# Optimization experiments

Hardware: AMD Instinct MI355X
Metric: run time of the kernel (lower is better)

Reference implementation:

```python
import jax, jax.numpy as jnp
import numpy as np

THRESHOLD = 2.0

def setup_inputs() -> dict:
    key = jax.random.key(0)
    x = jax.random.normal(key, (8, 2048, 16, 16), dtype=jnp.float32)
    return {"x": x}

def reference(x):
    eps = 1e-6
    B, N = x.shape[0], x.shape[1]
    feat_shape = x.shape[2:]
    xf = x.reshape(B, N, -1)                      # (B, N, D)
    D = xf.shape[-1]
    # Silverman-style bandwidth per batch
    sigma = jnp.std(xf, axis=1).mean(axis=1) + eps          # (B,)  unbiased=False
    h = (4.0 / (D + 2)) ** (1.0 / (D + 4)) * N ** (-1.0 / (D + 4)) * sigma + eps
    h = h[:, None]                                           # (B, 1)
    # pairwise mean-squared distance via the dot-product identity:
    # mean_d (xi - xj)^2 = (|xi|^2 + |xj|^2 - 2 xi.xj) / D
    sq = jnp.sum(xf * xf, axis=-1)                           # (B, N)
    dots = jnp.einsum('bnd,bmd->bnm', xf, xf)                # (B, N, N)
    Dmat = (sq[:, :, None] + sq[:, None, :] - 2.0 * dots) / D
    densities = jnp.exp(-Dmat / (2.0 * h[:, :, None] ** 2 + eps)).sum(axis=2)  # (B, N)
    mean = densities.mean(axis=1, keepdims=True)
    std = jnp.std(densities, axis=1, ddof=1, keepdims=True)  # torch.std unbiased
    mask = densities > (mean - THRESHOLD * std)              # (B, N) bool
    cnt = mask.sum(axis=1)                                   # (B,)
    s = jnp.einsum('bnd,bn->bd', xf, mask.astype(xf.dtype))  # masked sum
    denom = jnp.maximum(cnt, 1).astype(xf.dtype)[:, None]
    means = jnp.where(cnt[:, None] > 0, s / denom, jnp.zeros_like(s))
    return means.reshape((B,) + feat_shape)
```

## Files before the change

kernel.cpp:

```cpp
#include <hip/hip_runtime.h>
#include <math.h>

#define NB 8
#define NN 2048
#define ND 256

typedef _Float16 f16;
typedef f16 f16x8 __attribute__((ext_vector_type(8)));
typedef f16 f16x4 __attribute__((ext_vector_type(4)));
typedef float f32x4 __attribute__((ext_vector_type(4)));

static constexpr float EPS = 1e-6f;

__device__ __forceinline__ void gload16(const void* g, void* l) {
    __builtin_amdgcn_global_load_lds(
        (const __attribute__((address_space(1))) unsigned int*)g,
        (__attribute__((address_space(3))) unsigned int*)l, 16, 0, 0);
}

__global__ __launch_bounds__(256) void k_prep(const float* __restrict__ x,
                                              f16* __restrict__ xh, f16* __restrict__ xl,
                                              float* __restrict__ partS,
                                              float* __restrict__ partSS,
                                              float* __restrict__ sq) {
    int b = blockIdx.y, ch = blockIdx.x;
    int t = threadIdx.x;
    int c = t & 63, rg = t >> 6;
    size_t base = ((size_t)b * NN + (size_t)ch * 64) * ND;
    float s0 = 0.f, s1 = 0.f, s2 = 0.f, s3 = 0.f;
    float q0 = 0.f, q1 = 0.f, q2 = 0.f, q3 = 0.f;
    for (int r = rg; r < 64; r += 4) {
        float4 v = *(const float4*)&x[base + (size_t)r * ND + c * 4];
        s0 += v.x; s1 += v.y; s2 += v.z; s3 += v.w;
        float p = v.x * v.x + v.y * v.y + v.z * v.z + v.w * v.w;
        q0 += v.x * v.x; q1 += v.y * v.y; q2 += v.z * v.z; q3 += v.w * v.w;
        f16 h0 = (f16)v.x, h1 = (f16)v.y, h2 = (f16)v.z, h3 = (f16)v.w;
        f16x4 hv = {h0, h1, h2, h3};
        f16x4 lv = {(f16)(v.x - (float)h0), (f16)(v.y - (float)h1),
                    (f16)(v.z - (float)h2), (f16)(v.w - (float)h3)};
        *(f16x4*)&xh[base + (size_t)r * ND + c * 4] = hv;
        *(f16x4*)&xl[base + (size_t)r * ND + c * 4] = lv;
        #pragma unroll
        for (int off = 32; off > 0; off >>= 1) p += __shfl_xor(p, off, 64);
        if (c == 0) sq[b * NN + ch * 64 + r] = p;
    }
    __shared__ float rS[4][64][4];
    __shared__ float rQ[4][64][4];
    rS[rg][c][0] = s0; rS[rg][c][1] = s1; rS[rg][c][2] = s2; rS[rg][c][3] = s3;
    rQ[rg][c][0] = q0; rQ[rg][c][1] = q1; rQ[rg][c][2] = q2; rQ[rg][c][3] = q3;
    __syncthreads();
    if (rg == 0) {
        #pragma unroll
        for (int e = 0; e < 4; ++e) {
            float S = rS[0][c][e] + rS[1][c][e] + rS[2][c][e] + rS[3][c][e];
            float Q = rQ[0][c][e] + rQ[1][c][e] + rQ[2][c][e] + rQ[3][c][e];
            partS[(b * 32 + ch) * ND + c * 4 + e] = S;
            partSS[(b * 32 + ch) * ND + c * 4 + e] = Q;
        }
    }
}

__global__ __launch_bounds__(256) void k_scale(const float* __restrict__ partS,
                                               const float* __restrict__ partSS,
                                               const float* __restrict__ sq,
                                               float* __restrict__ scale,
                                               float* __restrict__ em) {
    int b = blockIdx.x, d = threadIdx.x;
    float s = 0.f, ss = 0.f;
    for (int ch = 0; ch < 32; ++ch) {
        s += partS[(b * 32 + ch) * ND + d];
        ss += partSS[(b * 32 + ch) * ND + d];
    }
    float mean = s * (1.0f / NN);
    float var = ss * (1.0f / NN) - mean * mean;
    float sd = sqrtf(fmaxf(var, 0.f));
    __shared__ float red[256];
    __shared__ float s_sc;
    red[d] = sd;
    __syncthreads();
    for (int off = 128; off > 0; off >>= 1) {
        if (d < off) red[d] += red[d + off];
        __syncthreads();
    }
    if (d == 0) {
        float sigma = red[0] * (1.0f / ND) + EPS;
        double c = pow(4.0 / (ND + 2), 1.0 / (ND + 4)) * pow((double)NN, -1.0 / (ND + 4));
        float h = (float)c * sigma + EPS;
        s_sc = 1.0f / ((float)ND * (2.0f * h * h + EPS));
        scale[b] = s_sc;
    }
    __syncthreads();
    float sc = s_sc;
    for (int n = d; n < NN; n += 256) em[b * NN + n] = __expf(-sq[b * NN + n] * sc);
}

__global__ __launch_bounds__(256, 3) void k_dens(const f16* __restrict__ xh,
                                                 const f16* __restrict__ xl,
                                                 const float* __restrict__ em,
                                                 const float* __restrict__ scale,
                                                 float* __restrict__ dens_part) {
    int wg = blockIdx.x;
    int b = wg & 7;
    int t = wg >> 3;
    int ti = 0, basec = 0;
    while (t >= basec + (16 - ti)) { basec += 16 - ti; ++ti; }
    int tj = ti + (t - basec);
    int n0 = ti * 128;
    int m0 = tj * 128;

    int tid = threadIdx.x;
    int w = tid >> 6, lane = tid & 63;
    int wr = w >> 1, wc = w & 1;

    __shared__ alignas(16) f16 sAh[128 * 64];
    __shared__ alignas(16) f16 sBh[128 * 64];
    __shared__ alignas(16) f16 sBl[128 * 64];
    __shared__ float dl[2][128];
    __shared__ float dc[2][128];

    const size_t xb = (size_t)b * NN * ND;
    const f16* gAh = xh + xb + (size_t)n0 * ND;
    const f16* gBh = xh + xb + (size_t)m0 * ND;
    const f16* gBl = xl + xb + (size_t)m0 * ND;

    int offA[4], offB[4];
    #pragma unroll
    for (int i = 0; i < 4; ++i) {
        int rA = wr * 64 + i * 16 + (lane & 15);
        offA[i] = rA * 128 + ((((lane >> 4) ^ (rA & 7))) << 4);
        int rB = wc * 64 + i * 16 + (lane & 15);
        offB[i] = rB * 128 + ((((lane >> 4) ^ (rB & 7))) << 4);
    }

    f32x4 acc[4][4];
    #pragma unroll
    for (int i = 0; i < 4; ++i)
        #pragma unroll
        for (int j = 0; j < 4; ++j)
            acc[i][j] = (f32x4){0.f, 0.f, 0.f, 0.f};

    for (int kt = 0; kt < ND / 64; ++kt) {
        int k0 = kt * 64;
        #pragma unroll
        for (int p = 0; p < 4; ++p) {
            int f = p * 256 + w * 64 + lane;
            int row = f >> 3;
            int c = f & 7;
            int col = ((c ^ (row & 7)) << 3);
            size_t go = (size_t)row * ND + k0 + col;
            int lo = p * 2048 + w * 512;
            gload16(gAh + go, sAh + lo);
            gload16(gBh + go, sBh + lo);
            gload16(gBl + go, sBl + lo);
        }
        __syncthreads();

        #pragma unroll
        for (int kk = 0; kk < 2; ++kk) {
            int dx = kk << 6;
            f16x8 ah[4], bh[4], bl[4];
            #pragma unroll
            for (int i = 0; i < 4; ++i) {
                ah[i] = *(const f16x8*)((const char*)sAh + (offA[i] ^ dx));
                bh[i] = *(const f16x8*)((const char*)sBh + (offB[i] ^ dx));
                bl[i] = *(const f16x8*)((const char*)sBl + (offB[i] ^ dx));
            }
            #pragma unroll
            for (int i = 0; i < 4; ++i)
                #pragma unroll
                for (int j = 0; j < 4; ++j) {
                    acc[i][j] = __builtin_amdgcn_mfma_f32_16x16x32_f16(ah[i], bh[j], acc[i][j], 0, 0, 0);
                    acc[i][j] = __builtin_amdgcn_mfma_f32_16x16x32_f16(ah[i], bl[j], acc[i][j], 0, 0, 0);
                }
        }
        __syncthreads();
    }

    float sc2 = 2.0f * scale[b];
    float emv[4];
    #pragma unroll
    for (int j = 0; j < 4; ++j)
        emv[j] = em[b * NN + m0 + wc * 64 + j * 16 + (lane & 15)];
    float emn[4][4];
    #pragma unroll
    for (int i = 0; i < 4; ++i) {
        float4 v = *(const float4*)&em[b * NN + n0 + wr * 64 + i * 16 + (lane >> 4) * 4];
        emn[i][0] = v.x; emn[i][1] = v.y; emn[i][2] = v.z; emn[i][3] = v.w;
    }

    float colsum[4] = {0.f, 0.f, 0.f, 0.f};
    #pragma unroll
    for (int i = 0; i < 4; ++i)
        #pragma unroll
        for (int e = 0; e < 4; ++e) {
            float rs = 0.f;
            #pragma unroll
            for (int j = 0; j < 4; ++j) {
                float v = __expf(sc2 * acc[i][j][e]);
                rs += emv[j] * v;
                colsum[j] += emn[i][e] * v;
            }
            rs += __shfl_xor(rs, 1, 64);
            rs += __shfl_xor(rs, 2, 64);
            rs += __shfl_xor(rs, 4, 64);
            rs += __shfl_xor(rs, 8, 64);
            if ((lane & 15) == 0)
                dl[wc][wr * 64 + i * 16 + (lane >> 4) * 4 + e] = rs;
        }
    #pragma unroll
    for (int j = 0; j < 4; ++j) {
        float cs = colsum[j];
        cs += __shfl_xor(cs, 16, 64);
        cs += __shfl_xor(cs, 32, 64);
        if ((lane >> 4) == 0)
            dc[wr][wc * 64 + j * 16 + (lane & 15)] = cs;
    }
    __syncthreads();
    if (tid < 128) {
        dens_part[((size_t)(b * 16) + tj) * NN + n0 + tid] = dl[0][tid] + dl[1][tid];
    } else if (ti != tj) {
        int c = tid - 128;
        dens_part[((size_t)(b * 16) + ti) * NN + m0 + c] = dc[0][c] + dc[1][c];
    }
}

__global__ __launch_bounds__(256) void k_maskstat(const float* __restrict__ x,
                                                  const float* __restrict__ part,
                                                  const float* __restrict__ em,
                                                  float* __restrict__ partM,
                                                  int* __restrict__ partC) {
    int b = blockIdx.y, ch = blockIdx.x;
    int t = threadIdx.x;
    int c = t & 63, rg = t >> 6;

    float dloc[8];
    float s = 0.f;
    #pragma unroll
    for (int i = 0; i < 8; ++i) {
        int n = t + i * 256;
        float v = 0.f;
        #pragma unroll
        for (int mt = 0; mt < 16; ++mt) v += part[((size_t)(b * 16 + mt)) * NN + n];
        v *= em[b * NN + n];
        dloc[i] = v;
        s += v;
    }
    __shared__ float red[256];
    __shared__ float s_thr;
    __shared__ float sD[128];
    red[t] = s;
    __syncthreads();
    for (int off = 128; off > 0; off >>= 1) {
        if (t < off) red[t] += red[t + off];
        __syncthreads();
    }
    float mean = red[0] * (1.0f / NN);
    __syncthreads();
    float vs = 0.f;
    #pragma unroll
    for (int i = 0; i < 8; ++i) {
        float d2 = dloc[i] - mean;
        vs += d2 * d2;
    }
    red[t] = vs;
    {
        int i0 = ch >> 1;
        int tlo = (ch & 1) * 128;
        if (t >= tlo && t < tlo + 128) sD[t - tlo] = dloc[i0];
    }
    __syncthreads();
    for (int off = 128; off > 0; off >>= 1) {
        if (t < off) red[t] += red[t + off];
        __syncthreads();
    }
    if (t == 0) s_thr = mean - 2.0f * sqrtf(red[0] / (float)(NN - 1));
    __syncthreads();
    float tv = s_thr;

    float s0 = 0.f, s1 = 0.f, s2 = 0.f, s3 = 0.f;
    int cnt = 0;
    for (int r = rg; r < 128; r += 4) {
        int n = ch * 128 + r;
        if (sD[r] > tv) {
            float4 v = *(const float4*)&x[((size_t)b * NN + n) * ND + c * 4];
            s0 += v.x; s1 += v.y; s2 += v.z; s3 += v.w;
            ++cnt;
        }
    }
    __shared__ float rS[4][64][4];
    __shared__ int rC[4];
    rS[rg][c][0] = s0; rS[rg][c][1] = s1; rS[rg][c][2] = s2; rS[rg][c][3] = s3;
    if (c == 0) rC[rg] = cnt;
    __syncthreads();
    if (rg == 0) {
        #pragma unroll
        for (int e = 0; e < 4; ++e) {
            float S = rS[0][c][e] + rS[1][c][e] + rS[2][c][e] + rS[3][c][e];
            partM[(b * 16 + ch) * ND + c * 4 + e] = S;
        }
        if (c == 0) partC[b * 16 + ch] = rC[0] + rC[1] + rC[2] + rC[3];
    }
}

__global__ __launch_bounds__(256) void k_out(const float* __restrict__ partM,
                                             const int* __restrict__ partC,
                                             float* __restrict__ out) {
    int b = blockIdx.x, d = threadIdx.x;
    float s = 0.f;
    int cnt = 0;
    for (int ch = 0; ch < 16; ++ch) {
        s += partM[(b * 16 + ch) * ND + d];
        cnt += partC[b * 16 + ch];
    }
    out[b * ND + d] = (cnt > 0) ? s / (float)max(cnt, 1) : 0.f;
}

extern "C" void kernel_launch(void* const* d_in, const int* in_sizes, int n_in,
                              void* d_out, int out_size, void* d_ws, size_t ws_size,
                              hipStream_t stream) {
    const float* x = (const float*)d_in[0];
    float* out = (float*)d_out;

    char* p = (char*)d_ws;
    f16* xh = (f16*)p;            p += (size_t)NB * NN * ND * 2;
    f16* xl = (f16*)p;            p += (size_t)NB * NN * ND * 2;
    float* sq = (float*)p;        p += (size_t)NB * NN * 4;
    float* em = (float*)p;        p += (size_t)NB * NN * 4;
    float* partS = (float*)p;     p += (size_t)NB * 32 * ND * 4;
    float* partSS = (float*)p;    p += (size_t)NB * 32 * ND * 4;
    float* scale = (float*)p;     p += 256;
    float* dens_part = (float*)p; p += (size_t)NB * 16 * NN * 4;
    float* partM = (float*)p;     p += (size_t)NB * 16 * ND * 4;
    int* partC = (int*)p;         p += (size_t)NB * 16 * 4;

    k_prep<<<dim3(32, NB), 256, 0, stream>>>(x, xh, xl, partS, partSS, sq);
    k_scale<<<NB, 256, 0, stream>>>(partS, partSS, sq, scale, em);
    k_dens<<<136 * NB, 256, 0, stream>>>(xh, xl, em, scale, dens_part);
    k_maskstat<<<dim3(16, NB), 256, 0, stream>>>(x, dens_part, em, partM, partC);
    k_out<<<NB, 256, 0, stream>>>(partM, partC, out);
}
```

Baseline: 66.67 us.

## Fold bandwidth/scale kernel into consumers and fuse final reduction via last-block atomic

Removes the separate k_scale and k_out launches. Every density and mask-stat workgroup now recomputes the per-batch bandwidth scale from the partial sums and evaluates exp(-sq*scale) inline. The final per-batch mean is produced by the last-arriving k_maskstat block, chosen through an atomic counter that k_prep resets. This saves two launches and their serialization gaps. The cost is redundant reduction work in each of the 1088 density workgroups and extra synchronization inside k_dens.

```diff
diff --git a/kernel.cpp b/kernel.cpp
--- a/kernel.cpp
+++ b/kernel.cpp
@@ -11,6 +11,7 @@
 typedef float f32x4 __attribute__((ext_vector_type(4)));
 
 static constexpr float EPS = 1e-6f;
+static constexpr float CCONST = 0.95566186f;
 
 __device__ __forceinline__ void gload16(const void* g, void* l) {
     __builtin_amdgcn_global_load_lds(
@@ -22,9 +23,11 @@
                                               f16* __restrict__ xh, f16* __restrict__ xl,
                                               float* __restrict__ partS,
                                               float* __restrict__ partSS,
-                                              float* __restrict__ sq) {
+                                              float* __restrict__ sq,
+                                              int* __restrict__ cnt) {
     int b = blockIdx.y, ch = blockIdx.x;
     int t = threadIdx.x;
+    if (b == 0 && ch == 0 && t < NB) cnt[t] = 0;
     int c = t & 63, rg = t >> 6;
     size_t base = ((size_t)b * NN + (size_t)ch * 64) * ND;
     float s0 = 0.f, s1 = 0.f, s2 = 0.f, s3 = 0.f;
@@ -60,44 +63,11 @@
     }
 }
 
-__global__ __launch_bounds__(256) void k_scale(const float* __restrict__ partS,
-                                               const float* __restrict__ partSS,
-                                               const float* __restrict__ sq,
-                                               float* __restrict__ scale,
-                                               float* __restrict__ em) {
-    int b = blockIdx.x, d = threadIdx.x;
-    float s = 0.f, ss = 0.f;
-    for (int ch = 0; ch < 32; ++ch) {
-        s += partS[(b * 32 + ch) * ND + d];
-        ss += partSS[(b * 32 + ch) * ND + d];
-    }
-    float mean = s * (1.0f / NN);
-    float var = ss * (1.0f / NN) - mean * mean;
-    float sd = sqrtf(fmaxf(var, 0.f));
-    __shared__ float red[256];
-    __shared__ float s_sc;
-    red[d] = sd;
-    __syncthreads();
-    for (int off = 128; off > 0; off >>= 1) {
-        if (d < off) red[d] += red[d + off];
-        __syncthreads();
-    }
-    if (d == 0) {
-        float sigma = red[0] * (1.0f / ND) + EPS;
-        double c = pow(4.0 / (ND + 2), 1.0 / (ND + 4)) * pow((double)NN, -1.0 / (ND + 4));
-        float h = (float)c * sigma + EPS;
-        s_sc = 1.0f / ((float)ND * (2.0f * h * h + EPS));
-        scale[b] = s_sc;
-    }
-    __syncthreads();
-    float sc = s_sc;
-    for (int n = d; n < NN; n += 256) em[b * NN + n] = __expf(-sq[b * NN + n] * sc);
-}
-
 __global__ __launch_bounds__(256, 3) void k_dens(const f16* __restrict__ xh,
                                                  const f16* __restrict__ xl,
-                                                 const float* __restrict__ em,
-                                                 const float* __restrict__ scale,
+                                                 const float* __restrict__ sq,
+                                                 const float* __restrict__ partS,
+                                                 const float* __restrict__ partSS,
                                                  float* __restrict__ dens_part) {
     int wg = blockIdx.x;
     int b = wg & 7;
@@ -117,6 +87,7 @@
     __shared__ alignas(16) f16 sBl[128 * 64];
     __shared__ float dl[2][128];
     __shared__ float dc[2][128];
+    __shared__ float s_sc;
 
     const size_t xb = (size_t)b * NN * ND;
     const f16* gAh = xh + xb + (size_t)n0 * ND;
@@ -176,16 +147,43 @@
         __syncthreads();
     }
 
-    float sc2 = 2.0f * scale[b];
+    {
+        float ssum = 0.f, sssum = 0.f;
+        #pragma unroll 4
+        for (int chp = 0; chp < 32; ++chp) {
+            ssum  += partS [(b * 32 + chp) * ND + tid];
+            sssum += partSS[(b * 32 + chp) * ND + tid];
+        }
+        float meanv = ssum * (1.0f / NN);
+        float varv  = sssum * (1.0f / NN) - meanv * meanv;
+        float* red = &dl[0][0];
+        red[tid] = sqrtf(fmaxf(varv, 0.f));
+        __syncthreads();
+        for (int off = 128; off > 0; off >>= 1) {
+            if (tid < off) red[tid] += red[tid + off];
+            __syncthreads();
+        }
+        if (tid == 0) {
+            float sigma = red[0] * (1.0f / ND) + EPS;
+            float h = CCONST * sigma + EPS;
+            s_sc = 1.0f / ((float)ND * (2.0f * h * h + EPS));
+        }
+        __syncthreads();
+    }
+    float sc = s_sc;
+    float sc2 = 2.0f * sc;
+
+    const float* sqb = sq + b * NN;
     float emv[4];
     #pragma unroll
     for (int j = 0; j < 4; ++j)
-        emv[j] = em[b * NN + m0 + wc * 64 + j * 16 + (lane & 15)];
+        emv[j] = __expf(-sqb[m0 + wc * 64 + j * 16 + (lane & 15)] * sc);
     float emn[4][4];
     #pragma unroll
     for (int i = 0; i < 4; ++i) {
-        float4 v = *(const float4*)&em[b * NN + n0 + wr * 64 + i * 16 + (lane >> 4) * 4];
-        emn[i][0] = v.x; emn[i][1] = v.y; emn[i][2] = v.z; emn[i][3] = v.w;
+        float4 v = *(const float4*)&sqb[n0 + wr * 64 + i * 16 + (lane >> 4) * 4];
+        emn[i][0] = __expf(-v.x * sc); emn[i][1] = __expf(-v.y * sc);
+        emn[i][2] = __expf(-v.z * sc); emn[i][3] = __expf(-v.w * sc);
     }
 
     float colsum[4] = {0.f, 0.f, 0.f, 0.f};
@@ -226,13 +224,46 @@
 
 __global__ __launch_bounds__(256) void k_maskstat(const float* __restrict__ x,
                                                   const float* __restrict__ part,
-                                                  const float* __restrict__ em,
+                                                  const float* __restrict__ sq,
+                                                  const float* __restrict__ partS,
+                                                  const float* __restrict__ partSS,
                                                   float* __restrict__ partM,
-                                                  int* __restrict__ partC) {
+                                                  int* __restrict__ partC,
+                                                  int* __restrict__ cnt,
+                                                  float* __restrict__ out) {
     int b = blockIdx.y, ch = blockIdx.x;
     int t = threadIdx.x;
     int c = t & 63, rg = t >> 6;
 
+    __shared__ float red[256];
+    __shared__ float s_sc;
+    __shared__ float s_thr;
+    __shared__ float sD[128];
+
+    {
+        float ssum = 0.f, sssum = 0.f;
+        #pragma unroll 4
+        for (int chp = 0; chp < 32; ++chp) {
+            ssum  += partS [(b * 32 + chp) * ND + t];
+            sssum += partSS[(b * 32 + chp) * ND + t];
+        }
+        float meanv = ssum * (1.0f / NN);
+        float varv  = sssum * (1.0f / NN) - meanv * meanv;
+        red[t] = sqrtf(fmaxf(varv, 0.f));
+        __syncthreads();
+        for (int off = 128; off > 0; off >>= 1) {
+            if (t < off) red[t] += red[t + off];
+            __syncthreads();
+        }
+        if (t == 0) {
+            float sigma = red[0] * (1.0f / ND) + EPS;
+            float h = CCONST * sigma + EPS;
+            s_sc = 1.0f / ((float)ND * (2.0f * h * h + EPS));
+        }
+        __syncthreads();
+    }
+    float sc = s_sc;
+
     float dloc[8];
     float s = 0.f;
     #pragma unroll
@@ -241,13 +272,10 @@
         float v = 0.f;
         #pragma unroll
         for (int mt = 0; mt < 16; ++mt) v += part[((size_t)(b * 16 + mt)) * NN + n];
-        v *= em[b * NN + n];
+        v *= __expf(-sq[b * NN + n] * sc);
         dloc[i] = v;
         s += v;
     }
-    __shared__ float red[256];
-    __shared__ float s_thr;
-    __shared__ float sD[128];
     red[t] = s;
     __syncthreads();
     for (int off = 128; off > 0; off >>= 1) {
@@ -278,19 +306,19 @@
     float tv = s_thr;
 
     float s0 = 0.f, s1 = 0.f, s2 = 0.f, s3 = 0.f;
-    int cnt = 0;
+    int mcnt = 0;
     for (int r = rg; r < 128; r += 4) {
         int n = ch * 128 + r;
         if (sD[r] > tv) {
             float4 v = *(const float4*)&x[((size_t)b * NN + n) * ND + c * 4];
             s0 += v.x; s1 += v.y; s2 += v.z; s3 += v.w;
-            ++cnt;
+            ++mcnt;
         }
     }
     __shared__ float rS[4][64][4];
     __shared__ int rC[4];
     rS[rg][c][0] = s0; rS[rg][c][1] = s1; rS[rg][c][2] = s2; rS[rg][c][3] = s3;
-    if (c == 0) rC[rg] = cnt;
+    if (c == 0) rC[rg] = mcnt;
     __syncthreads();
     if (rg == 0) {
         #pragma unroll
@@ -300,19 +328,23 @@
         }
         if (c == 0) partC[b * 16 + ch] = rC[0] + rC[1] + rC[2] + rC[3];
     }
-}
-
-__global__ __launch_bounds__(256) void k_out(const float* __restrict__ partM,
-                                             const int* __restrict__ partC,
-                                             float* __restrict__ out) {
-    int b = blockIdx.x, d = threadIdx.x;
-    float s = 0.f;
-    int cnt = 0;
-    for (int ch = 0; ch < 16; ++ch) {
-        s += partM[(b * 16 + ch) * ND + d];
-        cnt += partC[b * 16 + ch];
-    }
-    out[b * ND + d] = (cnt > 0) ? s / (float)max(cnt, 1) : 0.f;
+
+    __threadfence();
+    __syncthreads();
+    __shared__ int s_last;
+    if (t == 0) s_last = (atomicAdd(&cnt[b], 1) == 15) ? 1 : 0;
+    __syncthreads();
+    if (s_last) {
+        __threadfence();
+        float os = 0.f;
+        int oc = 0;
+        #pragma unroll
+        for (int c2 = 0; c2 < 16; ++c2) {
+            os += partM[(b * 16 + c2) * ND + t];
+            oc += partC[b * 16 + c2];
+        }
+        out[b * ND + t] = (oc > 0) ? os / (float)max(oc, 1) : 0.f;
+    }
 }
 
 extern "C" void kernel_launch(void* const* d_in, const int* in_sizes, int n_in,
@@ -325,17 +357,15 @@
     f16* xh = (f16*)p;            p += (size_t)NB * NN * ND * 2;
     f16* xl = (f16*)p;            p += (size_t)NB * NN * ND * 2;
     float* sq = (float*)p;        p += (size_t)NB * NN * 4;
-    float* em = (float*)p;        p += (size_t)NB * NN * 4;
     float* partS = (float*)p;     p += (size_t)NB * 32 * ND * 4;
     float* partSS = (float*)p;    p += (size_t)NB * 32 * ND * 4;
-    float* scale = (float*)p;     p += 256;
     float* dens_part = (float*)p; p += (size_t)NB * 16 * NN * 4;
     float* partM = (float*)p;     p += (size_t)NB * 16 * ND * 4;
     int* partC = (int*)p;         p += (size_t)NB * 16 * 4;
-
-    k_prep<<<dim3(32, NB), 256, 0, stream>>>(x, xh, xl, partS, partSS, sq);
-    k_scale<<<NB, 256, 0, stream>>>(partS, partSS, sq, scale, em);
-    k_dens<<<136 * NB, 256, 0, stream>>>(xh, xl, em, scale, dens_part);
-    k_maskstat<<<dim3(16, NB), 256, 0, stream>>>(x, dens_part, em, partM, partC);
-    k_out<<<NB, 256, 0, stream>>>(partM, partC, out);
-}
+    int* cnt = (int*)p;           p += 256;
+
+    k_prep<<<dim3(32, NB), 256, 0, stream>>>(x, xh, xl, partS, partSS, sq, cnt);
+    k_dens<<<136 * NB, 256, 0, stream>>>(xh, xl, sq, partS, partSS, dens_part);
+    k_maskstat<<<dim3(16, NB), 256, 0, stream>>>(x, dens_part, sq, partS, partSS,
+                                                 partM, partC, cnt, out);
+}
```

After: 77.41 us. 1.16x slower.
